# Kernel tuning notes

Measured on AMD Instinct MI355X. Metric: run time of the kernel, lower is better.

The kernel has to match this reference:

```python
import jax, jax.numpy as jnp
import numpy as np

V, N, D, R, L, KS = 32000, 2048, 1024, 16, 4, 7
B, H = 2, 4 * 1024
GMIN, GMAX, ACAP = 0.85, 1.0, 1.0


def rmsnorm(x, w, eps=1e-6):
    return x * jax.lax.rsqrt(jnp.mean(x * x, axis=-1, keepdims=True) + eps) * w


def l2norm(x, eps=1e-8):
    return x / jnp.maximum(jnp.linalg.norm(x, axis=-1, keepdims=True), eps)


def mlp(x, w1, b1, w2, b2):
    return jax.nn.gelu(x @ w1 + b1) @ w2 + b2


def k1_block(h, nw, w1, b1, w2, b2):
    return h + mlp(rmsnorm(h, nw), w1, b1, w2, b2)


def causal_conv(h, kernel):
    # depthwise causal conv with shared 1D kernel; kernel[0] = current step
    n = h.shape[1]
    hp = jnp.pad(h, ((0, 0), (KS - 1, 0), (0, 0)))
    out = jnp.zeros_like(h)
    for k in range(KS):  # KS is small & static
        out = out + kernel[k] * hp[:, KS - 1 - k: KS - 1 - k + n, :]
    return out


def k2_layer(h, p):
    (u, v, dlog, alog, glog, kern, pw, pb, n1w, n2w, w1, b1, w2, b2) = p
    residual = h
    hn = rmsnorm(h, n1w)
    gate = jax.nn.sigmoid(glog)
    out = gate * causal_conv(hn, kern)
    # low-rank q/k
    q = l2norm(hn @ u)          # (B,N,R)
    k = l2norm(hn @ v)          # (B,N,R)
    gamma = GMIN + (GMAX - GMIN) * jax.nn.sigmoid(dlog)   # (R,)
    alpha = ACAP * jax.nn.sigmoid(alog)                   # (R,)
    qa = q * alpha
    pos = jnp.arange(h.shape[1])
    diff = jnp.maximum(pos[:, None] - pos[None, :], 0).astype(h.dtype)
    mask = (pos[:, None] >= pos[None, :]).astype(h.dtype)
    # per-rank causal decay matrix gamma_r^(i-j): (R,N,N)
    decay = jnp.exp(diff[None] * jnp.log(gamma)[:, None, None]) * mask[None]
    scores = jnp.einsum('bir,rij,bjr->bij', qa, decay, k)  # (B,N,N)
    out = out + jnp.einsum('bij,bjd->bid', scores, hn)
    out = out @ pw + pb
    h = residual + out
    h = h + mlp(rmsnorm(h, n2w), w1, b1, w2, b2)
    return h


def setup_inputs() -> dict:
    key = jax.random.key(0)
    ks = jax.random.split(key, 32)
    f32 = jnp.float32
    inp = {
        'tokens': jax.random.randint(ks[0], (B, N), 0, V),
        'emb_table': jax.random.normal(ks[1], (V, D), f32) * 0.02,
        'k1a_nw': jnp.ones((D,), f32),
        'k1a_w1': jax.random.normal(ks[2], (D, H), f32) * 0.02,
        'k1a_b1': jnp.zeros((H,), f32),
        'k1a_w2': jax.random.normal(ks[3], (H, D), f32) * 0.02,
        'k1a_b2': jnp.zeros((D,), f32),
        'k2_u': jax.random.normal(ks[4], (L, D, R), f32) * 0.05,
        'k2_v': jax.random.normal(ks[5], (L, D, R), f32) * 0.05,
        'k2_dlog': jax.random.normal(ks[6], (L, R), f32) * 0.5,
        'k2_alog': jnp.zeros((L, R), f32),
        'k2_glog': jnp.zeros((L,), f32),
        'k2_kern': jax.random.normal(ks[7], (L, KS), f32) * 0.1,
        'k2_pw': jax.random.normal(ks[8], (L, D, D), f32) * 0.02,
        'k2_pb': jnp.zeros((L, D), f32),
        'k2_n1w': jnp.ones((L, D), f32),
        'k2_n2w': jnp.ones((L, D), f32),
        'k2_w1': jax.random.normal(ks[9], (L, D, H), f32) * 0.02,
        'k2_b1': jnp.zeros((L, H), f32),
        'k2_w2': jax.random.normal(ks[10], (L, H, D), f32) * 0.02,
        'k2_b2': jnp.zeros((L, D), f32),
        'k1b_nw': jnp.ones((D,), f32),
        'k1b_w1': jax.random.normal(ks[11], (D, H), f32) * 0.02,
        'k1b_b1': jnp.zeros((H,), f32),
        'k1b_w2': jax.random.normal(ks[12], (H, D), f32) * 0.02,
        'k1b_b2': jnp.zeros((D,), f32),
        'k0_nw': jnp.ones((D,), f32),
        'head_w': jax.random.normal(ks[13], (D, V), f32) * 0.02,
        'head_b': jnp.zeros((V,), f32),
    }
    return inp


def reference(tokens, emb_table,
              k1a_nw, k1a_w1, k1a_b1, k1a_w2, k1a_b2,
              k2_u, k2_v, k2_dlog, k2_alog, k2_glog, k2_kern,
              k2_pw, k2_pb, k2_n1w, k2_n2w, k2_w1, k2_b1, k2_w2, k2_b2,
              k1b_nw, k1b_w1, k1b_b1, k1b_w2, k1b_b2,
              k0_nw, head_w, head_b):
    h = emb_table[tokens]                                  # (B,N,D)
    h = k1_block(h, k1a_nw, k1a_w1, k1a_b1, k1a_w2, k1a_b2)
    stacked = (k2_u, k2_v, k2_dlog, k2_alog, k2_glog, k2_kern,
               k2_pw, k2_pb, k2_n1w, k2_n2w, k2_w1, k2_b1, k2_w2, k2_b2)
    def step(c, p):
        return k2_layer(c, p), None
    h, _ = jax.lax.scan(step, h, stacked)
    h = k1_block(h, k1b_nw, k1b_w1, k1b_b1, k1b_w2, k1b_b2)
    h = rmsnorm(h, k0_nw)                                  # K0 final norm
    return h @ head_w + head_b                             # (B,N,V)
```

## Files before the change

kernel.cpp:

```cpp
#include <hip/hip_runtime.h>
#include <hip/hip_bf16.h>

#define SEQ 2048
#define DIM 1024
#define RNK 16
#define NL 4
#define KT 7
#define BATCH 2
#define HID 4096
#define VOC 32000
#define BNROWS (BATCH*SEQ)
#define CHK 128
#define NCH (SEQ/CHK)
#define PRMS 128
#define KAPP 160

typedef __hip_bfloat16 bf16;
typedef __attribute__((ext_vector_type(8))) short bh8;
typedef __attribute__((ext_vector_type(4))) float vf4;

__device__ __forceinline__ float bfu(unsigned int u) { u <<= 16; return __builtin_bit_cast(float, u); }
__device__ __forceinline__ unsigned short f2bu(float x) { bf16 t = __float2bfloat16(x); return __builtin_bit_cast(unsigned short, t); }
__device__ __forceinline__ float b2f(bf16 x) { return __bfloat162float(x); }
__device__ __forceinline__ float sigm(float x) { return 1.f / (1.f + expf(-x)); }
__device__ __forceinline__ float gelu_t(float x) {
    float u = 0.7978845608028654f * (x + 0.044715f * x * x * x);
    return 0.5f * x * (1.f + tanhf(u));
}

__device__ __forceinline__ void gld16(const bf16* g, bf16* l) {
    __builtin_amdgcn_global_load_lds(
        (const __attribute__((address_space(1))) void*)g,
        (__attribute__((address_space(3))) void*)l,
        16, 0, 0);
}

__global__ void embed_kernel(const int* __restrict__ tokens, const float* __restrict__ emb,
                             float* __restrict__ h) {
    int row = blockIdx.x;
    int tok = tokens[row];
    const float4* src = (const float4*)(emb + (size_t)tok * DIM);
    float4* dst = (float4*)(h + (size_t)row * DIM);
    dst[threadIdx.x] = src[threadIdx.x];
}

__global__ void rmsnorm_kernel(const float* __restrict__ in, const float* __restrict__ wt,
                               bf16* __restrict__ out) {
    int row = blockIdx.x;
    int tx = threadIdx.x;
    float4 v = ((const float4*)(in + (size_t)row * DIM))[tx];
    float ss = v.x * v.x + v.y * v.y + v.z * v.z + v.w * v.w;
#pragma unroll
    for (int off = 32; off > 0; off >>= 1) ss += __shfl_down(ss, off);
    __shared__ float red[4];
    int lane = tx & 63, wv = tx >> 6;
    if (lane == 0) red[wv] = ss;
    __syncthreads();
    float tot = red[0] + red[1] + red[2] + red[3];
    float scale = rsqrtf(tot * (1.f / DIM) + 1e-6f);
    float4 w4 = ((const float4*)wt)[tx];
    uint2 o;
    o.x = f2bu(v.x * scale * w4.x) | ((unsigned int)f2bu(v.y * scale * w4.y) << 16);
    o.y = f2bu(v.z * scale * w4.z) | ((unsigned int)f2bu(v.w * scale * w4.w) << 16);
    *(uint2*)(out + (size_t)row * DIM + tx * 4) = o;
}

__global__ void transpose_cast_kernel(const float* __restrict__ in, bf16* __restrict__ out,
                                      int K, int Nc) {
    __shared__ float tile[32][33];
    int n0 = blockIdx.x * 32, k0 = blockIdx.y * 32;
    int tx = threadIdx.x & 31, ty = threadIdx.x >> 5;
#pragma unroll
    for (int i = 0; i < 32; i += 8)
        tile[ty + i][tx] = in[(size_t)(k0 + ty + i) * Nc + n0 + tx];
    __syncthreads();
#pragma unroll
    for (int i = 0; i < 32; i += 8)
        out[(size_t)(n0 + ty + i) * K + k0 + tx] = __float2bfloat16(tile[tx][ty + i]);
}

__global__ void prep_kernel(const float* __restrict__ dlog, const float* __restrict__ alog,
                            const float* __restrict__ glog, const float* __restrict__ kern,
                            float* __restrict__ prm) {
    int l = blockIdx.x, t = threadIdx.x;
    float* p = prm + l * PRMS;
    if (t < RNK) {
        float g = 0.85f + 0.15f * sigm(dlog[l * RNK + t]);
        float lg = logf(g);
        p[t] = g;
        p[16 + t] = lg;
        p[32 + t] = expf(lg * (float)CHK);
        p[48 + t] = sigm(alog[l * RNK + t]);
    }
    if (t < KT) {
        float gate = sigm(glog[l]);
        p[64 + t] = gate * kern[l * KT + t];
    }
}

__global__ void prep_uv_kernel(const float* __restrict__ u, const float* __restrict__ v,
                               bf16* __restrict__ uvT) {
    int l = blockIdx.y;
    int k = blockIdx.x * 256 + threadIdx.x;
    const float* ul = u + (size_t)l * DIM * RNK;
    const float* vl = v + (size_t)l * DIM * RNK;
    bf16* o = uvT + (size_t)l * 32 * DIM;
#pragma unroll
    for (int r = 0; r < RNK; ++r) {
        o[(size_t)r * DIM + k] = __float2bfloat16(ul[(size_t)k * RNK + r]);
        o[(size_t)(RNK + r) * DIM + k] = __float2bfloat16(vl[(size_t)k * RNK + r]);
    }
}

__global__ void conv_kernel(const bf16* __restrict__ hn, const float* __restrict__ prm,
                            float* __restrict__ Z) {
    int t = blockIdx.x * 256 + threadIdx.x;
    int d4 = (t & 255) * 4;
    int row = t >> 8;
    int n = row & (SEQ - 1);
    float a0 = 0, a1 = 0, a2 = 0, a3 = 0;
#pragma unroll
    for (int kk = 0; kk < KT; ++kk) {
        if (n - kk < 0) break;
        float wv = prm[64 + kk];
        uint2 hv = *(const uint2*)(hn + (size_t)(row - kk) * DIM + d4);
        a0 += wv * bfu(hv.x & 0xffffu);
        a1 += wv * bfu(hv.x >> 16);
        a2 += wv * bfu(hv.y & 0xffffu);
        a3 += wv * bfu(hv.y >> 16);
    }
    float4 o = {a0, a1, a2, a3};
    *(float4*)(Z + (size_t)row * DIM + d4) = o;
}

__global__ __launch_bounds__(64)
void qk_mfma_kernel(const bf16* __restrict__ hn, const bf16* __restrict__ uvT,
                    const float* __restrict__ prm, float* __restrict__ qa,
                    float* __restrict__ kn) {
    int row0 = blockIdx.x * 32;
    int lane = threadIdx.x;
    int fr = lane & 15, kf = (lane >> 4) * 8;
    vf4 acc[2][2] = {};
#pragma unroll 4
    for (int kt = 0; kt < DIM / 32; ++kt) {
        int k0 = kt * 32;
        bh8 b0 = *(const bh8*)(uvT + (size_t)fr * DIM + k0 + kf);
        bh8 b1 = *(const bh8*)(uvT + (size_t)(16 + fr) * DIM + k0 + kf);
        bh8 a0 = *(const bh8*)(hn + (size_t)(row0 + fr) * DIM + k0 + kf);
        bh8 a1 = *(const bh8*)(hn + (size_t)(row0 + 16 + fr) * DIM + k0 + kf);
        acc[0][0] = __builtin_amdgcn_mfma_f32_16x16x32_bf16(a0, b0, acc[0][0], 0, 0, 0);
        acc[0][1] = __builtin_amdgcn_mfma_f32_16x16x32_bf16(a0, b1, acc[0][1], 0, 0, 0);
        acc[1][0] = __builtin_amdgcn_mfma_f32_16x16x32_bf16(a1, b0, acc[1][0], 0, 0, 0);
        acc[1][1] = __builtin_amdgcn_mfma_f32_16x16x32_bf16(a1, b1, acc[1][1], 0, 0, 0);
    }
    int fq = lane >> 4;
    float alpha = prm[48 + fr];
#pragma unroll
    for (int m = 0; m < 2; ++m) {
#pragma unroll
        for (int j = 0; j < 4; ++j) {
            float qv = acc[m][0][j], kv = acc[m][1][j];
            float sq = qv * qv, sk = kv * kv;
#pragma unroll
            for (int mask = 1; mask < 16; mask <<= 1) {
                sq += __shfl_xor(sq, mask);
                sk += __shfl_xor(sk, mask);
            }
            int row = row0 + m * 16 + fq * 4 + j;
            qa[(size_t)row * RNK + fr] = qv / fmaxf(sqrtf(sq), 1e-8f) * alpha;
            kn[(size_t)row * RNK + fr] = kv / fmaxf(sqrtf(sk), 1e-8f);
        }
    }
}

__global__ void trans_hn_kernel(const bf16* __restrict__ hn, bf16* __restrict__ HB) {
    __shared__ bf16 tile[32][40];
    int bc = blockIdx.x;
    int d0 = blockIdx.y * 32, j0 = blockIdx.z * 32;
    int tx = threadIdx.x & 31, ty = threadIdx.x >> 5;
    size_t rowb = (size_t)bc * CHK;
#pragma unroll
    for (int i = 0; i < 32; i += 8)
        tile[ty + i][tx] = hn[(rowb + j0 + ty + i) * DIM + d0 + tx];
    __syncthreads();
    bf16* Hp = HB + (size_t)bc * DIM * KAPP;
#pragma unroll
    for (int i = 0; i < 32; i += 8)
        Hp[(size_t)(d0 + ty + i) * KAPP + j0 + tx] = tile[tx][ty + i];
}

__global__ void scores_kernel(const float* __restrict__ qa, const float* __restrict__ kn,
                              const float* __restrict__ prm, bf16* __restrict__ SA,
                              bf16* __restrict__ kdtB) {
    int bc = blockIdx.x;
    __shared__ float ptab[CHK][16];
    for (int e = threadIdx.x; e < CHK * 16; e += 256) {
        int tt = e >> 4, r = e & 15;
        ptab[tt][r] = expf(prm[16 + r] * (float)tt);
    }
    __syncthreads();
    size_t rowb = (size_t)bc * CHK;
    bf16* SAp = SA + (size_t)bc * CHK * KAPP;
    for (int e = threadIdx.x; e < CHK * CHK; e += 256) {
        int i = e >> 7, j = e & (CHK - 1);
        float vsum = 0.f;
        if (i >= j) {
            const float* qp = qa + (rowb + i) * RNK;
            const float* kp = kn + (rowb + j) * RNK;
#pragma unroll
            for (int r = 0; r < 16; ++r) vsum += qp[r] * ptab[i - j][r] * kp[r];
        }
        SAp[(size_t)i * KAPP + j] = __float2bfloat16(vsum);
    }
    for (int e = threadIdx.x; e < CHK * 32; e += 256) {
        int i = e >> 5, rr = e & 31;
        float w = 0.f;
        if (rr < 16) w = qa[(rowb + i) * RNK + rr] * expf(prm[16 + rr] * (float)(i + 1));
        SAp[(size_t)i * KAPP + CHK + rr] = __float2bfloat16(w);
    }
    bf16* kp2 = kdtB + (size_t)bc * RNK * CHK;
    for (int e = threadIdx.x; e < RNK * CHK; e += 256) {
        int r = e >> 7, j = e & (CHK - 1);
        kp2[e] = __float2bfloat16(ptab[CHK - 1 - j][r] * kn[(rowb + j) * RNK + r]);
    }
}

__global__ __launch_bounds__(64)
void chunkU_kernel(const bf16* __restrict__ HB, const bf16* __restrict__ kdtB,
                   float* __restrict__ U) {
    int bc = blockIdx.x;
    int d0 = blockIdx.y * 64;
    int lane = threadIdx.x;
    int fr = lane & 15, kf = (lane >> 4) * 8;
    const bf16* Hp = HB + (size_t)bc * DIM * KAPP;
    const bf16* Kp = kdtB + (size_t)bc * RNK * CHK;
    vf4 acc[4] = {};
#pragma unroll
    for (int kt = 0; kt < 4; ++kt) {
        int k0 = kt * 32;
        bh8 bb = *(const bh8*)(Kp + (size_t)fr * CHK + k0 + kf);
#pragma unroll
        for (int m = 0; m < 4; ++m) {
            bh8 a = *(const bh8*)(Hp + (size_t)(d0 + m * 16 + fr) * KAPP + k0 + kf);
            acc[m] = __builtin_amdgcn_mfma_f32_16x16x32_bf16(a, bb, acc[m], 0, 0, 0);
        }
    }
    int fq = lane >> 4;
    float* Up = U + (size_t)bc * DIM * RNK;
#pragma unroll
    for (int m = 0; m < 4; ++m)
#pragma unroll
        for (int j = 0; j < 4; ++j)
            Up[(size_t)(d0 + m * 16 + fq * 4 + j) * RNK + fr] = acc[m][j];
}

__global__ void scanP_kernel(const float* __restrict__ U, const float* __restrict__ prm,
                             bf16* __restrict__ HB) {
    int g = blockIdx.x * 256 + threadIdx.x;
    int d = g & (DIM - 1);
    int b = g >> 10;
    float gC[16], p[16];
#pragma unroll
    for (int r = 0; r < 16; ++r) { gC[r] = prm[32 + r]; p[r] = 0.f; }
    for (int c = 0; c < NCH; ++c) {
        int bc = b * NCH + c;
        unsigned int pk[8];
#pragma unroll
        for (int q = 0; q < 8; ++q)
            pk[q] = (unsigned int)f2bu(p[2 * q]) | ((unsigned int)f2bu(p[2 * q + 1]) << 16);
        uint4* dst = (uint4*)(HB + (size_t)bc * DIM * KAPP + (size_t)d * KAPP + CHK);
        dst[0] = make_uint4(pk[0], pk[1], pk[2], pk[3]);
        dst[1] = make_uint4(pk[4], pk[5], pk[6], pk[7]);
        const float4* up = (const float4*)(U + ((size_t)bc * DIM + d) * RNK);
#pragma unroll
        for (int q = 0; q < 4; ++q) {
            float4 u4 = up[q];
            p[4 * q + 0] = gC[4 * q + 0] * p[4 * q + 0] + u4.x;
            p[4 * q + 1] = gC[4 * q + 1] * p[4 * q + 1] + u4.y;
            p[4 * q + 2] = gC[4 * q + 2] * p[4 * q + 2] + u4.z;
            p[4 * q + 3] = gC[4 * q + 3] * p[4 * q + 3] + u4.w;
        }
    }
}

__global__ __launch_bounds__(256)
void apply_gemm_kernel(const bf16* __restrict__ SA, const bf16* __restrict__ HB,
                       const float* __restrict__ Z, bf16* __restrict__ Zb) {
    __shared__ alignas(16) bf16 As[128][40];
    __shared__ alignas(16) bf16 Bs[128][40];
    int bc = blockIdx.y;
    int colB0 = blockIdx.x * 128;
    int t = threadIdx.x;
    int lane = t & 63, wid = t >> 6;
    int wr = wid >> 1, wc = wid & 1;
    vf4 acc[4][4] = {};
    const bf16* A = SA + (size_t)bc * CHK * KAPP;
    const bf16* BT = HB + (size_t)bc * DIM * KAPP;
    int r1 = t >> 2, ko1 = (t & 3) * 8;
    int fr = lane & 15, kf = (lane >> 4) * 8;
#pragma unroll
    for (int kt = 0; kt < 5; ++kt) {
        int k0 = kt * 32;
        int4 va1 = *(const int4*)(A + (size_t)r1 * KAPP + k0 + ko1);
        int4 va2 = *(const int4*)(A + (size_t)(r1 + 64) * KAPP + k0 + ko1);
        int4 vb1 = *(const int4*)(BT + (size_t)(colB0 + r1) * KAPP + k0 + ko1);
        int4 vb2 = *(const int4*)(BT + (size_t)(colB0 + r1 + 64) * KAPP + k0 + ko1);
        __syncthreads();
        *(int4*)&As[r1][ko1] = va1;
        *(int4*)&As[r1 + 64][ko1] = va2;
        *(int4*)&Bs[r1][ko1] = vb1;
        *(int4*)&Bs[r1 + 64][ko1] = vb2;
        __syncthreads();
        bh8 a[4], bb[4];
#pragma unroll
        for (int m = 0; m < 4; ++m) a[m] = *(const bh8*)&As[wr * 64 + m * 16 + fr][kf];
#pragma unroll
        for (int n = 0; n < 4; ++n) bb[n] = *(const bh8*)&Bs[wc * 64 + n * 16 + fr][kf];
#pragma unroll
        for (int m = 0; m < 4; ++m)
#pragma unroll
            for (int n = 0; n < 4; ++n)
                acc[m][n] = __builtin_amdgcn_mfma_f32_16x16x32_bf16(a[m], bb[n], acc[m][n], 0, 0, 0);
    }
    int fq = lane >> 4;
    size_t rowb = (size_t)bc * CHK;
#pragma unroll
    for (int m = 0; m < 4; ++m) {
#pragma unroll
        for (int n = 0; n < 4; ++n) {
            int col = colB0 + wc * 64 + n * 16 + fr;
#pragma unroll
            for (int j = 0; j < 4; ++j) {
                size_t row = rowb + wr * 64 + m * 16 + fq * 4 + j;
                size_t idx = row * DIM + col;
                Zb[idx] = __float2bfloat16(Z[idx] + acc[m][n][j]);
            }
        }
    }
}

template <int EPI>
__global__ __launch_bounds__(256)
void gemm_kernel(const bf16* __restrict__ A, const bf16* __restrict__ BT,
                 const float* __restrict__ bias, const float* __restrict__ res,
                 float* __restrict__ outF, bf16* __restrict__ outB,
                 int M, int Nc, int K, int lda) {
    __shared__ alignas(16) bf16 As[128][32];
    __shared__ alignas(16) bf16 Bs[128][32];
    int gx = gridDim.x;
    int orig = blockIdx.y * gx + blockIdx.x;
    int qch = (gx * gridDim.y) >> 3;
    int wg = (orig & 7) * qch + (orig >> 3);
    int bn = wg % gx, bm = wg / gx;
    int t = threadIdx.x;
    int lane = t & 63, wid = t >> 6;
    int wr = wid >> 1, wc = wid & 1;
    vf4 acc[4][4] = {};
    const int rowA0 = bm * 128, colB0 = bn * 128;
    int fr = lane & 15, kf = (lane >> 4) * 8;
    int c0 = wid * 2;
    int lrow = lane >> 2;
    int lcol = (lane & 3) * 8;
    const bf16* Ag0 = A + (size_t)(rowA0 + c0 * 16 + lrow) * lda + lcol;
    const bf16* Ag1 = A + (size_t)(rowA0 + c0 * 16 + 16 + lrow) * lda + lcol;
    const bf16* Bg0 = BT + (size_t)(colB0 + c0 * 16 + lrow) * lda + lcol;
    const bf16* Bg1 = BT + (size_t)(colB0 + c0 * 16 + 16 + lrow) * lda + lcol;
    bf16* Al0 = &As[0][0] + c0 * 512;
    bf16* Al1 = Al0 + 512;
    bf16* Bl0 = &Bs[0][0] + c0 * 512;
    bf16* Bl1 = Bl0 + 512;
    int nk = K >> 5;
    for (int kt = 0; kt < nk; ++kt) {
        int k0 = kt * 32;
        __syncthreads();
        gld16(Ag0 + k0, Al0);
        gld16(Ag1 + k0, Al1);
        gld16(Bg0 + k0, Bl0);
        gld16(Bg1 + k0, Bl1);
        asm volatile("s_waitcnt vmcnt(0)" ::: "memory");
        __syncthreads();
        bh8 a[4], bb[4];
#pragma unroll
        for (int m = 0; m < 4; ++m) a[m] = *(const bh8*)&As[wr * 64 + m * 16 + fr][kf];
#pragma unroll
        for (int n = 0; n < 4; ++n) bb[n] = *(const bh8*)&Bs[wc * 64 + n * 16 + fr][kf];
#pragma unroll
        for (int m = 0; m < 4; ++m)
#pragma unroll
            for (int n = 0; n < 4; ++n)
                acc[m][n] = __builtin_amdgcn_mfma_f32_16x16x32_bf16(a[m], bb[n], acc[m][n], 0, 0, 0);
    }
    int fq = lane >> 4;
#pragma unroll
    for (int m = 0; m < 4; ++m) {
#pragma unroll
        for (int n = 0; n < 4; ++n) {
            int col = colB0 + wc * 64 + n * 16 + fr;
            float bv = bias[col];
#pragma unroll
            for (int j = 0; j < 4; ++j) {
                int row = rowA0 + wr * 64 + m * 16 + fq * 4 + j;
                size_t idx = (size_t)row * Nc + col;
                float v2 = acc[m][n][j] + bv;
                if (EPI == 1) v2 += res[idx];
                outF[idx] = v2;
            }
        }
    }
}

#define SB __builtin_amdgcn_sched_barrier(0)
template <int EPI>
__global__ __launch_bounds__(512, 2)
void gemm256_kernel(const bf16* __restrict__ A, const bf16* __restrict__ BT,
                    const float* __restrict__ bias,
                    float* __restrict__ outF, bf16* __restrict__ outB,
                    int M, int Nc, int K, int lda) {
    extern __shared__ char smem[];
    bf16* Alds = (bf16*)smem;
    bf16* Blds = (bf16*)(smem + 65536);
    if (EPI == 3) {
        size_t zo = (size_t)blockIdx.z * K;
        A += zo; BT += zo;
        outF += (size_t)blockIdx.z * ((size_t)M * Nc);
    }
    int gx = gridDim.x;
    int orig = blockIdx.y * gx + blockIdx.x;
    int qch = (gx * gridDim.y) >> 3;
    int wg = (orig & 7) * qch + (orig >> 3);
    int bn = wg % gx, bm = wg / gx;
    int rowA0 = bm * 256, colB0 = bn * 256;
    int tid = threadIdx.x;
    int lane = tid & 63, wid = tid >> 6;
    int wm = wid >> 2, wn = wid & 3;
    int fr = lane & 15;
    int kf8 = ((((lane >> 4) & 3) ^ ((fr >> 1) & 3)) * 8);
    int srow = wid * 16 + (lane >> 2);
    int scol = (((lane & 3) ^ ((lane >> 3) & 3)) * 8);
    const bf16* Ags = A + (size_t)(rowA0 + srow) * lda + scol;
    const bf16* Bgs = BT + (size_t)(colB0 + srow) * lda + scol;
    int sbase = wid * 512;
    auto stA = [&](int d, int kh, int k0) {
        bf16* dst = Alds + (d * 2 + kh) * 8192 + sbase;
        const bf16* src = Ags + k0 + kh * 32;
        gld16(src, dst);
        gld16(src + (size_t)128 * lda, dst + 4096);
    };
    auto stB = [&](int d, int kh, int k0) {
        bf16* dst = Blds + (d * 2 + kh) * 8192 + sbase;
        const bf16* src = Bgs + k0 + kh * 32;
        gld16(src, dst);
        gld16(src + (size_t)128 * lda, dst + 4096);
    };
    const bf16* Ard = Alds + (size_t)(wm * 128 + fr) * 32 + kf8;
    const bf16* Brd = Blds + (size_t)(wn * 64 + fr) * 32 + kf8;
    vf4 acc[8][4] = {};
    int nt = K >> 6;
    stA(0, 0, 0); stB(0, 0, 0); stA(0, 1, 0); stB(0, 1, 0);
    for (int t = 0; t < nt; ++t) {
        int d = t & 1, nd = d ^ 1;
        int k1 = (t + 1) << 6;
        bool pf = (t + 1 < nt);
        int dof = d * 16384;
        bh8 bF[4];
        if (pf) { stA(nd, 0, k1); asm volatile("s_waitcnt vmcnt(6)" ::: "memory"); }
        else    {                 asm volatile("s_waitcnt vmcnt(4)" ::: "memory"); }
        SB; __builtin_amdgcn_s_barrier(); SB;
        {
            bh8 a0 = *(const bh8*)(Ard + dof + 0 * 512);
            bh8 a1 = *(const bh8*)(Ard + dof + 1 * 512);
            bh8 a2 = *(const bh8*)(Ard + dof + 2 * 512);
            bh8 a3 = *(const bh8*)(Ard + dof + 3 * 512);
#pragma unroll
            for (int n = 0; n < 4; ++n) bF[n] = *(const bh8*)(Brd + dof + n * 512);
            __builtin_amdgcn_s_setprio(1);
#pragma unroll
            for (int n = 0; n < 4; ++n) {
                acc[0][n] = __builtin_amdgcn_mfma_f32_16x16x32_bf16(a0, bF[n], acc[0][n], 0, 0, 0);
                acc[1][n] = __builtin_amdgcn_mfma_f32_16x16x32_bf16(a1, bF[n], acc[1][n], 0, 0, 0);
                acc[2][n] = __builtin_amdgcn_mfma_f32_16x16x32_bf16(a2, bF[n], acc[2][n], 0, 0, 0);
                acc[3][n] = __builtin_amdgcn_mfma_f32_16x16x32_bf16(a3, bF[n], acc[3][n], 0, 0, 0);
            }
            __builtin_amdgcn_s_setprio(0);
        }
        SB;
        if (pf) stB(nd, 0, k1);
        SB; __builtin_amdgcn_s_barrier(); SB;
        {
            bh8 a0 = *(const bh8*)(Ard + dof + 4 * 512);
            bh8 a1 = *(const bh8*)(Ard + dof + 5 * 512);
            bh8 a2 = *(const bh8*)(Ard + dof + 6 * 512);
            bh8 a3 = *(const bh8*)(Ard + dof + 7 * 512);
            __builtin_amdgcn_s_setprio(1);
#pragma unroll
            for (int n = 0; n < 4; ++n) {
                acc[4][n] = __builtin_amdgcn_mfma_f32_16x16x32_bf16(a0, bF[n], acc[4][n], 0, 0, 0);
                acc[5][n] = __builtin_amdgcn_mfma_f32_16x16x32_bf16(a1, bF[n], acc[5][n], 0, 0, 0);
                acc[6][n] = __builtin_amdgcn_mfma_f32_16x16x32_bf16(a2, bF[n], acc[6][n], 0, 0, 0);
                acc[7][n] = __builtin_amdgcn_mfma_f32_16x16x32_bf16(a3, bF[n], acc[7][n], 0, 0, 0);
            }
            __builtin_amdgcn_s_setprio(0);
        }
        SB;
        int dof1 = dof + 8192;
        if (pf) { stA(nd, 1, k1); asm volatile("s_waitcnt vmcnt(6)" ::: "memory"); }
        else    {                 asm volatile("s_waitcnt vmcnt(0)" ::: "memory"); }
        SB; __builtin_amdgcn_s_barrier(); SB;
        {
            bh8 a0 = *(const bh8*)(Ard + dof1 + 0 * 512);
            bh8 a1 = *(const bh8*)(Ard + dof1 + 1 * 512);
            bh8 a2 = *(const bh8*)(Ard + dof1 + 2 * 512);
            bh8 a3 = *(const bh8*)(Ard + dof1 + 3 * 512);
#pragma unroll
            for (int n = 0; n < 4; ++n) bF[n] = *(const bh8*)(Brd + dof1 + n * 512);
            __builtin_amdgcn_s_setprio(1);
#pragma unroll
            for (int n = 0; n < 4; ++n) {
                acc[0][n] = __builtin_amdgcn_mfma_f32_16x16x32_bf16(a0, bF[n], acc[0][n], 0, 0, 0);
                acc[1][n] = __builtin_amdgcn_mfma_f32_16x16x32_bf16(a1, bF[n], acc[1][n], 0, 0, 0);
                acc[2][n] = __builtin_amdgcn_mfma_f32_16x16x32_bf16(a2, bF[n], acc[2][n], 0, 0, 0);
                acc[3][n] = __builtin_amdgcn_mfma_f32_16x16x32_bf16(a3, bF[n], acc[3][n], 0, 0, 0);
            }
            __builtin_amdgcn_s_setprio(0);
        }
        SB;
        if (pf) stB(nd, 1, k1);
        SB; __builtin_amdgcn_s_barrier(); SB;
        {
            bh8 a0 = *(const bh8*)(Ard + dof1 + 4 * 512);
            bh8 a1 = *(const bh8*)(Ard + dof1 + 5 * 512);
            bh8 a2 = *(const bh8*)(Ard + dof1 + 6 * 512);
            bh8 a3 = *(const bh8*)(Ard + dof1 + 7 * 512);
            __builtin_amdgcn_s_setprio(1);
#pragma unroll
            for (int n = 0; n < 4; ++n) {
                acc[4][n] = __builtin_amdgcn_mfma_f32_16x16x32_bf16(a0, bF[n], acc[4][n], 0, 0, 0);
                acc[5][n] = __builtin_amdgcn_mfma_f32_16x16x32_bf16(a1, bF[n], acc[5][n], 0, 0, 0);
                acc[6][n] = __builtin_amdgcn_mfma_f32_16x16x32_bf16(a2, bF[n], acc[6][n], 0, 0, 0);
                acc[7][n] = __builtin_amdgcn_mfma_f32_16x16x32_bf16(a3, bF[n], acc[7][n], 0, 0, 0);
            }
            __builtin_amdgcn_s_setprio(0);
        }
        SB;
    }
    int fq = lane >> 4;
#pragma unroll
    for (int mi = 0; mi < 8; ++mi) {
#pragma unroll
        for (int ni = 0; ni < 4; ++ni) {
            int col = colB0 + wn * 64 + ni * 16 + fr;
            float bv = (EPI == 3) ? 0.f : bias[col];
#pragma unroll
            for (int j = 0; j < 4; ++j) {
                int row = rowA0 + wm * 128 + mi * 16 + fq * 4 + j;
                size_t idx = (size_t)row * Nc + col;
                float v2 = acc[mi][ni][j] + bv;
                if (EPI == 2) outB[idx] = __float2bfloat16(gelu_t(v2));
                else outF[idx] = v2;
            }
        }
    }
}

__global__ void combine4_kernel(const float* __restrict__ P, const float* __restrict__ bias,
                                float* __restrict__ h) {
    int t = blockIdx.x * 256 + threadIdx.x;
    int col4 = t & (DIM / 4 - 1);
    const size_t S = (size_t)BNROWS * DIM;
    float4 p0 = ((const float4*)P)[t];
    float4 p1 = ((const float4*)(P + S))[t];
    float4 p2 = ((const float4*)(P + 2 * S))[t];
    float4 p3 = ((const float4*)(P + 3 * S))[t];
    float4 bv = ((const float4*)bias)[col4];
    float4 hv = ((float4*)h)[t];
    hv.x += (p0.x + p1.x) + (p2.x + p3.x) + bv.x;
    hv.y += (p0.y + p1.y) + (p2.y + p3.y) + bv.y;
    hv.z += (p0.z + p1.z) + (p2.z + p3.z) + bv.z;
    hv.w += (p0.w + p1.w) + (p2.w + p3.w) + bv.w;
    ((float4*)h)[t] = hv;
}

extern "C" void kernel_launch(void* const* d_in, const int* in_sizes, int n_in,
                              void* d_out, int out_size, void* d_ws, size_t ws_size,
                              hipStream_t stream) {
    (void)in_sizes; (void)n_in; (void)out_size; (void)ws_size;
    const int* tokens = (const int*)d_in[0];
    const float* emb = (const float*)d_in[1];
    const float* k1a_nw = (const float*)d_in[2];
    const float* k1a_w1 = (const float*)d_in[3];
    const float* k1a_b1 = (const float*)d_in[4];
    const float* k1a_w2 = (const float*)d_in[5];
    const float* k1a_b2 = (const float*)d_in[6];
    const float* k2_u = (const float*)d_in[7];
    const float* k2_v = (const float*)d_in[8];
    const float* k2_dlog = (const float*)d_in[9];
    const float* k2_alog = (const float*)d_in[10];
    const float* k2_glog = (const float*)d_in[11];
    const float* k2_kern = (const float*)d_in[12];
    const float* k2_pw = (const float*)d_in[13];
    const float* k2_pb = (const float*)d_in[14];
    const float* k2_n1w = (const float*)d_in[15];
    const float* k2_n2w = (const float*)d_in[16];
    const float* k2_w1 = (const float*)d_in[17];
    const float* k2_b1 = (const float*)d_in[18];
    const float* k2_w2 = (const float*)d_in[19];
    const float* k2_b2 = (const float*)d_in[20];
    const float* k1b_nw = (const float*)d_in[21];
    const float* k1b_w1 = (const float*)d_in[22];
    const float* k1b_b1 = (const float*)d_in[23];
    const float* k1b_w2 = (const float*)d_in[24];
    const float* k1b_b2 = (const float*)d_in[25];
    const float* k0_nw = (const float*)d_in[26];
    const float* head_w = (const float*)d_in[27];
    const float* head_b = (const float*)d_in[28];
    float* out = (float*)d_out;

    (void)hipFuncSetAttribute((const void*)gemm256_kernel<0>,
                              hipFuncAttributeMaxDynamicSharedMemorySize, 131072);
    (void)hipFuncSetAttribute((const void*)gemm256_kernel<2>,
                              hipFuncAttributeMaxDynamicSharedMemorySize, 131072);
    (void)hipFuncSetAttribute((const void*)gemm256_kernel<3>,
                              hipFuncAttributeMaxDynamicSharedMemorySize, 131072);

    char* wsp = (char*)d_ws;
    auto alloc = [&](size_t bytes) -> char* {
        char* p = wsp;
        wsp += (bytes + 255) & ~(size_t)255;
        return p;
    };
    float* h   = (float*)alloc((size_t)BNROWS * DIM * 4);
    float* Z   = (float*)alloc((size_t)BNROWS * DIM * 4);
    bf16* hnb  = (bf16*)alloc((size_t)BNROWS * DIM * 2);
    bf16* Zb   = (bf16*)alloc((size_t)BNROWS * DIM * 2);
    bf16* t1b  = (bf16*)alloc((size_t)BNROWS * HID * 2);
    float* qaB = (float*)alloc((size_t)BNROWS * RNK * 4);
    float* knB = (float*)alloc((size_t)BNROWS * RNK * 4);
    float* U   = (float*)alloc((size_t)BATCH * NCH * DIM * RNK * 4);
    bf16* HB   = (bf16*)alloc((size_t)BATCH * NCH * DIM * KAPP * 2);
    bf16* SA   = (bf16*)alloc((size_t)BATCH * NCH * CHK * KAPP * 2);
    bf16* kdtB = (bf16*)alloc((size_t)BATCH * NCH * RNK * CHK * 2);
    float* prm = (float*)alloc((size_t)NL * PRMS * 4);
    bf16* uvT  = (bf16*)alloc((size_t)NL * 32 * DIM * 2);
    bf16* w1aT = (bf16*)alloc((size_t)HID * DIM * 2);
    bf16* w2aT = (bf16*)alloc((size_t)DIM * HID * 2);
    bf16* w1bT = (bf16*)alloc((size_t)HID * DIM * 2);
    bf16* w2bT = (bf16*)alloc((size_t)DIM * HID * 2);
    bf16* pwT  = (bf16*)alloc((size_t)NL * DIM * DIM * 2);
    bf16* w1T  = (bf16*)alloc((size_t)NL * DIM * HID * 2);
    bf16* w2T  = (bf16*)alloc((size_t)NL * HID * DIM * 2);
    bf16* headT = (bf16*)alloc((size_t)VOC * DIM * 2);
    float* Pk  = (float*)alloc((size_t)4 * BNROWS * DIM * 4);

    hipMemsetAsync(HB, 0, (size_t)BATCH * NCH * DIM * KAPP * 2, stream);

    auto T = [&](const float* in, bf16* o, int K, int Nc) {
        transpose_cast_kernel<<<dim3(Nc / 32, K / 32), 256, 0, stream>>>(in, o, K, Nc);
    };
    T(k1a_w1, w1aT, DIM, HID);
    T(k1a_w2, w2aT, HID, DIM);
    T(k1b_w1, w1bT, DIM, HID);
    T(k1b_w2, w2bT, HID, DIM);
    for (int l = 0; l < NL; ++l) {
        T(k2_pw + (size_t)l * DIM * DIM, pwT + (size_t)l * DIM * DIM, DIM, DIM);
        T(k2_w1 + (size_t)l * DIM * HID, w1T + (size_t)l * DIM * HID, DIM, HID);
        T(k2_w2 + (size_t)l * HID * DIM, w2T + (size_t)l * HID * DIM, HID, DIM);
    }
    T(head_w, headT, DIM, VOC);
    prep_kernel<<<NL, 32, 0, stream>>>(k2_dlog, k2_alog, k2_glog, k2_kern, prm);
    prep_uv_kernel<<<dim3(DIM / 256, NL), 256, 0, stream>>>(k2_u, k2_v, uvT);

    auto mlp_block = [&](const float* nw, const bf16* W1, const float* B1,
                         const bf16* W2, const float* B2) {
        rmsnorm_kernel<<<BNROWS, 256, 0, stream>>>(h, nw, hnb);
        gemm256_kernel<2><<<dim3(HID / 256, BNROWS / 256), 512, 131072, stream>>>(
            hnb, W1, B1, nullptr, t1b, BNROWS, HID, DIM, DIM);
        gemm256_kernel<3><<<dim3(DIM / 256, BNROWS / 256, 4), 512, 131072, stream>>>(
            t1b, W2, nullptr, Pk, nullptr, BNROWS, DIM, HID / 4, HID);
        combine4_kernel<<<BNROWS * DIM / 4 / 256, 256, 0, stream>>>(Pk, B2, h);
    };

    embed_kernel<<<BNROWS, 256, 0, stream>>>(tokens, emb, h);
    mlp_block(k1a_nw, w1aT, k1a_b1, w2aT, k1a_b2);

    for (int l = 0; l < NL; ++l) {
        const float* prm_l = prm + l * PRMS;
        rmsnorm_kernel<<<BNROWS, 256, 0, stream>>>(h, k2_n1w + (size_t)l * DIM, hnb);
        conv_kernel<<<BNROWS, 256, 0, stream>>>(hnb, prm_l, Z);
        qk_mfma_kernel<<<BNROWS / 32, 64, 0, stream>>>(hnb, uvT + (size_t)l * 32 * DIM,
                                                       prm_l, qaB, knB);
        trans_hn_kernel<<<dim3(BATCH * NCH, DIM / 32, CHK / 32), 256, 0, stream>>>(hnb, HB);
        scores_kernel<<<BATCH * NCH, 256, 0, stream>>>(qaB, knB, prm_l, SA, kdtB);
        chunkU_kernel<<<dim3(BATCH * NCH, DIM / 64), 64, 0, stream>>>(HB, kdtB, U);
        scanP_kernel<<<BATCH * DIM / 256, 256, 0, stream>>>(U, prm_l, HB);
        apply_gemm_kernel<<<dim3(DIM / 128, BATCH * NCH), 256, 0, stream>>>(SA, HB, Z, Zb);
        gemm_kernel<1><<<dim3(DIM / 128, BNROWS / 128), 256, 0, stream>>>(
            Zb, pwT + (size_t)l * DIM * DIM, k2_pb + (size_t)l * DIM, h, h, nullptr,
            BNROWS, DIM, DIM, DIM);
        mlp_block(k2_n2w + (size_t)l * DIM, w1T + (size_t)l * DIM * HID, k2_b1 + (size_t)l * HID,
                  w2T + (size_t)l * HID * DIM, k2_b2 + (size_t)l * DIM);
    }

    mlp_block(k1b_nw, w1bT, k1b_b1, w2bT, k1b_b2);

    rmsnorm_kernel<<<BNROWS, 256, 0, stream>>>(h, k0_nw, hnb);
    gemm256_kernel<0><<<dim3(VOC / 256, BNROWS / 256), 512, 131072, stream>>>(
        hnb, headT, head_b, out, nullptr, BNROWS, VOC, DIM, DIM);
}
```

Measured before the change: 1.710 ms.

## Fuse split-K combine with next RMSNorm and swap GEMM tile raster order

The split-K reduction kernel after each MLP now also computes the row RMSNorm for the following stage and writes the bf16 normalized activations, which removes six separate rmsnorm launches and their extra read of h. The fused kernel runs one block per row, so it needs a block-level reduction with a barrier. Separately, gemm256 block remapping now walks the M dimension fastest instead of N, which changes which tiles run together and how A and B tiles are reused in L2.

```diff
diff --git a/kernel.cpp b/kernel.cpp
--- a/kernel.cpp
+++ b/kernel.cpp
@@ -424,11 +424,11 @@
         A += zo; BT += zo;
         outF += (size_t)blockIdx.z * ((size_t)M * Nc);
     }
-    int gx = gridDim.x;
+    int gx = gridDim.x, gy = gridDim.y;
     int orig = blockIdx.y * gx + blockIdx.x;
-    int qch = (gx * gridDim.y) >> 3;
+    int qch = (gx * gy) >> 3;
     int wg = (orig & 7) * qch + (orig >> 3);
-    int bn = wg % gx, bm = wg / gx;
+    int bm = wg % gy, bn = wg / gy;
     int rowA0 = bm * 256, colB0 = bn * 256;
     int tid = threadIdx.x;
     int lane = tid & 63, wid = tid >> 6;
@@ -562,22 +562,38 @@
     }
 }
 
-__global__ void combine4_kernel(const float* __restrict__ P, const float* __restrict__ bias,
-                                float* __restrict__ h) {
-    int t = blockIdx.x * 256 + threadIdx.x;
-    int col4 = t & (DIM / 4 - 1);
+__global__ void combine4_norm_kernel(const float* __restrict__ P, const float* __restrict__ bias,
+                                     const float* __restrict__ nw, float* __restrict__ h,
+                                     bf16* __restrict__ hnb) {
+    int row = blockIdx.x;
+    int tx = threadIdx.x;
+    int t = row * 256 + tx;
     const size_t S = (size_t)BNROWS * DIM;
     float4 p0 = ((const float4*)P)[t];
     float4 p1 = ((const float4*)(P + S))[t];
     float4 p2 = ((const float4*)(P + 2 * S))[t];
     float4 p3 = ((const float4*)(P + 3 * S))[t];
-    float4 bv = ((const float4*)bias)[col4];
+    float4 bv = ((const float4*)bias)[tx];
     float4 hv = ((float4*)h)[t];
     hv.x += (p0.x + p1.x) + (p2.x + p3.x) + bv.x;
     hv.y += (p0.y + p1.y) + (p2.y + p3.y) + bv.y;
     hv.z += (p0.z + p1.z) + (p2.z + p3.z) + bv.z;
     hv.w += (p0.w + p1.w) + (p2.w + p3.w) + bv.w;
     ((float4*)h)[t] = hv;
+    float ss = hv.x * hv.x + hv.y * hv.y + hv.z * hv.z + hv.w * hv.w;
+#pragma unroll
+    for (int off = 32; off > 0; off >>= 1) ss += __shfl_down(ss, off);
+    __shared__ float red[4];
+    int lane = tx & 63, wv = tx >> 6;
+    if (lane == 0) red[wv] = ss;
+    __syncthreads();
+    float tot = red[0] + red[1] + red[2] + red[3];
+    float scale = rsqrtf(tot * (1.f / DIM) + 1e-6f);
+    float4 w4 = ((const float4*)nw)[tx];
+    uint2 o;
+    o.x = f2bu(hv.x * scale * w4.x) | ((unsigned int)f2bu(hv.y * scale * w4.y) << 16);
+    o.y = f2bu(hv.z * scale * w4.z) | ((unsigned int)f2bu(hv.w * scale * w4.w) << 16);
+    *(uint2*)(hnb + (size_t)row * DIM + tx * 4) = o;
 }
 
 extern "C" void kernel_launch(void* const* d_in, const int* in_sizes, int n_in,
@@ -669,22 +685,21 @@
     prep_kernel<<<NL, 32, 0, stream>>>(k2_dlog, k2_alog, k2_glog, k2_kern, prm);
     prep_uv_kernel<<<dim3(DIM / 256, NL), 256, 0, stream>>>(k2_u, k2_v, uvT);
 
-    auto mlp_block = [&](const float* nw, const bf16* W1, const float* B1,
-                         const bf16* W2, const float* B2) {
-        rmsnorm_kernel<<<BNROWS, 256, 0, stream>>>(h, nw, hnb);
+    auto mlp_core = [&](const bf16* W1, const float* B1, const bf16* W2, const float* B2,
+                        const float* nw_next) {
         gemm256_kernel<2><<<dim3(HID / 256, BNROWS / 256), 512, 131072, stream>>>(
             hnb, W1, B1, nullptr, t1b, BNROWS, HID, DIM, DIM);
         gemm256_kernel<3><<<dim3(DIM / 256, BNROWS / 256, 4), 512, 131072, stream>>>(
             t1b, W2, nullptr, Pk, nullptr, BNROWS, DIM, HID / 4, HID);
-        combine4_kernel<<<BNROWS * DIM / 4 / 256, 256, 0, stream>>>(Pk, B2, h);
+        combine4_norm_kernel<<<BNROWS, 256, 0, stream>>>(Pk, B2, nw_next, h, hnb);
     };
 
     embed_kernel<<<BNROWS, 256, 0, stream>>>(tokens, emb, h);
-    mlp_block(k1a_nw, w1aT, k1a_b1, w2aT, k1a_b2);
+    rmsnorm_kernel<<<BNROWS, 256, 0, stream>>>(h, k1a_nw, hnb);
+    mlp_core(w1aT, k1a_b1, w2aT, k1a_b2, k2_n1w);
 
     for (int l = 0; l < NL; ++l) {
         const float* prm_l = prm + l * PRMS;
-        rmsnorm_kernel<<<BNROWS, 256, 0, stream>>>(h, k2_n1w + (size_t)l * DIM, hnb);
         conv_kernel<<<BNROWS, 256, 0, stream>>>(hnb, prm_l, Z);
         qk_mfma_kernel<<<BNROWS / 32, 64, 0, stream>>>(hnb, uvT + (size_t)l * 32 * DIM,
                                                        prm_l, qaB, knB);
@@ -696,13 +711,14 @@
         gemm_kernel<1><<<dim3(DIM / 128, BNROWS / 128), 256, 0, stream>>>(
             Zb, pwT + (size_t)l * DIM * DIM, k2_pb + (size_t)l * DIM, h, h, nullptr,
             BNROWS, DIM, DIM, DIM);
-        mlp_block(k2_n2w + (size_t)l * DIM, w1T + (size_t)l * DIM * HID, k2_b1 + (size_t)l * HID,
-                  w2T + (size_t)l * HID * DIM, k2_b2 + (size_t)l * DIM);
-    }
-
-    mlp_block(k1b_nw, w1bT, k1b_b1, w2bT, k1b_b2);
-
-    rmsnorm_kernel<<<BNROWS, 256, 0, stream>>>(h, k0_nw, hnb);
+        rmsnorm_kernel<<<BNROWS, 256, 0, stream>>>(h, k2_n2w + (size_t)l * DIM, hnb);
+        const float* nw_next = (l < NL - 1) ? (k2_n1w + (size_t)(l + 1) * DIM) : k1b_nw;
+        mlp_core(w1T + (size_t)l * DIM * HID, k2_b1 + (size_t)l * HID,
+                 w2T + (size_t)l * HID * DIM, k2_b2 + (size_t)l * DIM, nw_next);
+    }
+
+    mlp_core(w1bT, k1b_b1, w2bT, k1b_b2, k0_nw);
+
     gemm256_kernel<0><<<dim3(VOC / 256, BNROWS / 256), 512, 131072, stream>>>(
         hnb, headT, head_b, out, nullptr, BNROWS, VOC, DIM, DIM);
 }
```

After: 1.711 ms. About the same (+0.1%).
